# Performance work log

Hardware: AMD Instinct MI355X
Metric: run time of the kernel (lower is better)

## Reference

```python
import jax, jax.numpy as jnp
import numpy as np
import math

D_MODEL = 1024
N_HEADS = 16
D_K = 64
D_V = 64
B = 4
S = 1024


def setup_inputs() -> dict:
    key = jax.random.key(0)
    ks = jax.random.split(key, 11)
    # xavier-ish init scale for projections
    s_in = 1.0 / math.sqrt(D_MODEL)
    return {
        "queries": jax.random.normal(ks[0], (B, S, D_MODEL), jnp.float32),
        "keys": jax.random.normal(ks[1], (B, S, D_MODEL), jnp.float32),
        "values": jax.random.normal(ks[2], (B, S, D_MODEL), jnp.float32),
        "Wq": jax.random.normal(ks[3], (D_MODEL, N_HEADS * D_K), jnp.float32) * s_in,
        "bq": jnp.zeros((N_HEADS * D_K,), jnp.float32),
        "Wk": jax.random.normal(ks[4], (D_MODEL, N_HEADS * D_K), jnp.float32) * s_in,
        "bk": jnp.zeros((N_HEADS * D_K,), jnp.float32),
        "Wv": jax.random.normal(ks[5], (D_MODEL, N_HEADS * D_V), jnp.float32) * s_in,
        "bv": jnp.zeros((N_HEADS * D_V,), jnp.float32),
        "Wo": jax.random.normal(ks[6], (N_HEADS * D_V, D_MODEL), jnp.float32) * (1.0 / math.sqrt(N_HEADS * D_V)),
        "bo": jnp.zeros((D_MODEL,), jnp.float32),
    }


def reference(queries, keys, values, Wq, bq, Wk, bk, Wv, bv, Wo, bo):
    Bq, Sq, _ = queries.shape
    Sk = keys.shape[1]
    scale = 1.0 / math.sqrt(D_K)
    # projections -> [B, S, H, d]
    q = (queries @ Wq + bq).reshape(Bq, Sq, N_HEADS, D_K)
    k = (keys @ Wk + bk).reshape(Bq, Sk, N_HEADS, D_K)
    v = (values @ Wv + bv).reshape(Bq, Sk, N_HEADS, D_V)
    # scaled dot-product attention: scores [B, H, Sq, Sk]
    scores = jnp.einsum("bqhd,bkhd->bhqk", q, k) * scale
    attn = jax.nn.softmax(scores, axis=-1)
    # weighted values -> [B, Sq, H*D_V]
    out = jnp.einsum("bhqk,bkhd->bqhd", attn, v).reshape(Bq, Sq, N_HEADS * D_V)
    return out @ Wo + bo
```

## Files before the change

kernel.cpp:

```cpp
#include <hip/hip_runtime.h>

typedef __bf16 bf16;
typedef __attribute__((ext_vector_type(4))) __bf16 bf16x4;
typedef __attribute__((ext_vector_type(8))) __bf16 bf16x8;
typedef __attribute__((ext_vector_type(4))) float f32x4;

#define D_MODEL 1024
#define NH      16
#define DHEAD   64
#define BATCH   4
#define SLEN    1024
#define MROWS   (BATCH * SLEN)
#define C2SCALE 0.18033688f
#define SOFTMAX_OFF 20.0f

__device__ __forceinline__ void async_load16(const void* g, void* l) {
  __builtin_amdgcn_global_load_lds(
      (const __attribute__((address_space(1))) unsigned int*)g,
      (__attribute__((address_space(3))) unsigned int*)l,
      16, 0, 0);
}

__global__ __launch_bounds__(256) void cast3_kernel(
    const float* __restrict__ x0, const float* __restrict__ x1, const float* __restrict__ x2,
    bf16* __restrict__ y0, bf16* __restrict__ y1, bf16* __restrict__ y2, int n)
{
  const float* x; bf16* y;
  switch (blockIdx.y) {
    case 0: x = x0; y = y0; break;
    case 1: x = x1; y = y1; break;
    default: x = x2; y = y2; break;
  }
  int i = (blockIdx.x * 256 + threadIdx.x) * 4;
  if (i + 3 < n) {
    f32x4 v = *(const f32x4*)(x + i);
    bf16x4 o;
    o[0] = (bf16)v[0]; o[1] = (bf16)v[1]; o[2] = (bf16)v[2]; o[3] = (bf16)v[3];
    *(bf16x4*)(y + i) = o;
  }
}

__global__ __launch_bounds__(256) void transpose_cast4_kernel(
    const float* __restrict__ w0, const float* __restrict__ w1,
    const float* __restrict__ w2, const float* __restrict__ w3,
    bf16* __restrict__ t0, bf16* __restrict__ t1,
    bf16* __restrict__ t2, bf16* __restrict__ t3)
{
  __shared__ float tile[32][33];
  const float* W; bf16* T;
  switch (blockIdx.z) {
    case 0: W = w0; T = t0; break;
    case 1: W = w1; T = t1; break;
    case 2: W = w2; T = t2; break;
    default: W = w3; T = t3; break;
  }
  const int bx = blockIdx.x * 32, by = blockIdx.y * 32;
  const int tx = threadIdx.x & 31, ty = threadIdx.x >> 5;
  #pragma unroll
  for (int i = 0; i < 32; i += 8)
    tile[ty + i][tx] = W[(size_t)(by + ty + i) * 1024 + bx + tx];
  __syncthreads();
  #pragma unroll
  for (int i = 0; i < 32; i += 8)
    T[(size_t)(bx + ty + i) * 1024 + by + tx] = (bf16)tile[tx][ty + i];
}

__global__ __launch_bounds__(256) void proj_qkv_kernel(
    const bf16* __restrict__ Xq, const bf16* __restrict__ Xk, const bf16* __restrict__ Xv,
    const bf16* __restrict__ WqT, const bf16* __restrict__ WkT, const bf16* __restrict__ WvT,
    const float* __restrict__ bq, const float* __restrict__ bk, const float* __restrict__ bv,
    bf16* __restrict__ Qh, bf16* __restrict__ Kh, bf16* __restrict__ VTo)
{
  __shared__ bf16 As[128 * 32];
  __shared__ bf16 Bs[128 * 32];
  const int z = blockIdx.z;
  const bf16 *A, *BT; const float* bias;
  switch (z) {
    case 0: A = Xq; BT = WqT; bias = bq; break;
    case 1: A = Xk; BT = WkT; bias = bk; break;
    default: A = Xv; BT = WvT; bias = bv; break;
  }
  const int t = threadIdx.x;
  const int wave = t >> 6, lane = t & 63;
  const int quad = lane >> 4, l16 = lane & 15;
  const int wr = wave >> 1, wc = wave & 1;
  const int bM = blockIdx.y * 128, bN = blockIdx.x * 128;

  f32x4 acc[4][4] = {};

  for (int k0 = 0; k0 < D_MODEL; k0 += 32) {
    __syncthreads();
    #pragma unroll
    for (int i = 0; i < 2; ++i) {
      const int idx = i * 256 + t;
      const int row = idx >> 2, cg = idx & 3;
      async_load16(A  + (size_t)(bM + row) * D_MODEL + k0 + cg * 8,
                   As + (size_t)(i * 256 + wave * 64) * 8);
      async_load16(BT + (size_t)(bN + row) * D_MODEL + k0 + cg * 8,
                   Bs + (size_t)(i * 256 + wave * 64) * 8);
    }
    __syncthreads();

    bf16x8 af[4], bfr[4];
    #pragma unroll
    for (int i = 0; i < 4; ++i)
      af[i] = *(const bf16x8*)(As + (wr * 64 + i * 16 + l16) * 32 + quad * 8);
    #pragma unroll
    for (int j = 0; j < 4; ++j)
      bfr[j] = *(const bf16x8*)(Bs + (wc * 64 + j * 16 + l16) * 32 + quad * 8);
    #pragma unroll
    for (int i = 0; i < 4; ++i)
      #pragma unroll
      for (int j = 0; j < 4; ++j)
        acc[i][j] = __builtin_amdgcn_mfma_f32_16x16x32_bf16(af[i], bfr[j], acc[i][j], 0, 0, 0);
  }

  #pragma unroll
  for (int j = 0; j < 4; ++j) {
    const int col = bN + wc * 64 + j * 16 + l16;
    const int h = col >> 6, d = col & 63;
    const float bv_ = bias[col];
    #pragma unroll
    for (int i = 0; i < 4; ++i) {
      const int row0 = bM + wr * 64 + i * 16 + quad * 4;
      const int b = row0 >> 10, s0 = row0 & 1023;
      if (z == 0) {
        bf16* dst = Qh + ((size_t)(b * NH + h) * SLEN) * DHEAD;
        #pragma unroll
        for (int r = 0; r < 4; ++r)
          dst[(size_t)(s0 + r) * DHEAD + d] = (bf16)((acc[i][j][r] + bv_) * C2SCALE);
      } else if (z == 1) {
        bf16* dst = Kh + ((size_t)(b * NH + h) * SLEN) * DHEAD;
        #pragma unroll
        for (int r = 0; r < 4; ++r)
          dst[(size_t)(s0 + r) * DHEAD + d] = (bf16)(acc[i][j][r] + bv_);
      } else {
        bf16x4 pv;
        #pragma unroll
        for (int r = 0; r < 4; ++r) pv[r] = (bf16)(acc[i][j][r] + bv_);
        *(bf16x4*)(VTo + ((size_t)(b * NH + h) * DHEAD + d) * SLEN + s0) = pv;
      }
    }
  }
}

__global__ __launch_bounds__(256) void out_proj_kernel(
    const bf16* __restrict__ AO, const bf16* __restrict__ WoT,
    const float* __restrict__ bo, float* __restrict__ Out)
{
  __shared__ bf16 As[64 * 32];
  __shared__ bf16 Bs[128 * 32];
  const int t = threadIdx.x;
  const int wave = t >> 6, lane = t & 63;
  const int quad = lane >> 4, l16 = lane & 15;
  const int wr = wave >> 1, wc = wave & 1;
  const int bM = blockIdx.y * 64, bN = blockIdx.x * 128;

  f32x4 acc[2][4] = {};

  for (int k0 = 0; k0 < D_MODEL; k0 += 32) {
    __syncthreads();
    {
      const int row = t >> 2, cg = t & 3;
      async_load16(AO  + (size_t)(bM + row) * D_MODEL + k0 + cg * 8,
                   As + (size_t)(wave * 64) * 8);
    }
    #pragma unroll
    for (int i = 0; i < 2; ++i) {
      const int idx = i * 256 + t;
      const int row = idx >> 2, cg = idx & 3;
      async_load16(WoT + (size_t)(bN + row) * D_MODEL + k0 + cg * 8,
                   Bs + (size_t)(i * 256 + wave * 64) * 8);
    }
    __syncthreads();

    bf16x8 af[2], bfr[4];
    #pragma unroll
    for (int i = 0; i < 2; ++i)
      af[i] = *(const bf16x8*)(As + (wr * 32 + i * 16 + l16) * 32 + quad * 8);
    #pragma unroll
    for (int j = 0; j < 4; ++j)
      bfr[j] = *(const bf16x8*)(Bs + (wc * 64 + j * 16 + l16) * 32 + quad * 8);
    #pragma unroll
    for (int i = 0; i < 2; ++i)
      #pragma unroll
      for (int j = 0; j < 4; ++j)
        acc[i][j] = __builtin_amdgcn_mfma_f32_16x16x32_bf16(af[i], bfr[j], acc[i][j], 0, 0, 0);
  }

  #pragma unroll
  for (int j = 0; j < 4; ++j) {
    const int col = bN + wc * 64 + j * 16 + l16;
    const float bv_ = bo[col];
    #pragma unroll
    for (int i = 0; i < 2; ++i) {
      const int row0 = bM + wr * 32 + i * 16 + quad * 4;
      #pragma unroll
      for (int r = 0; r < 4; ++r)
        Out[(size_t)(row0 + r) * D_MODEL + col] = acc[i][j][r] + bv_;
    }
  }
}

#define OCS  68
#define WSEG (32 * OCS)
__global__ __launch_bounds__(256) void attn_kernel(
    const bf16* __restrict__ Q, const bf16* __restrict__ K,
    const bf16* __restrict__ VT, bf16* __restrict__ O)
{
  const int bh = blockIdx.y;
  const int b = bh >> 4, h = bh & 15;
  const int qBase = blockIdx.x * 32;

  __shared__ float smem_f[4 * WSEG + 4 * 32];

  const int t = threadIdx.x;
  const int wave = t >> 6, lane = t & 63;
  const int quad = lane >> 4, l16 = lane & 15;
  const int kt0 = wave * 256;

  const bf16* qb = Q  + (size_t)bh * SLEN * DHEAD;
  const bf16* kb = K  + (size_t)bh * SLEN * DHEAD;
  const bf16* vb = VT + (size_t)bh * DHEAD * SLEN;

  bf16x8 qa[2][2];
  #pragma unroll
  for (int g = 0; g < 2; ++g) {
    const bf16* qr = qb + (size_t)(qBase + g * 16 + l16) * DHEAD;
    qa[g][0] = *(const bf16x8*)(qr + quad * 8);
    qa[g][1] = *(const bf16x8*)(qr + 32 + quad * 8);
  }

  f32x4 o_acc[2][4] = {};
  float rs[2][4] = {};

  bf16* Pw = (bf16*)smem_f + wave * (2 * 16 * 72);

  bf16x8 kf0[4], kf1[4];
  #pragma unroll
  for (int jn = 0; jn < 4; ++jn) {
    const bf16* kr = kb + (size_t)(kt0 + jn * 16 + l16) * DHEAD;
    kf0[jn] = *(const bf16x8*)(kr + quad * 8);
    kf1[jn] = *(const bf16x8*)(kr + 32 + quad * 8);
  }

  #pragma unroll
  for (int tt = 0; tt < 4; ++tt) {
    const int kt = kt0 + tt * 64;

    bf16x8 vf0[4], vf1[4];
    #pragma unroll
    for (int jn = 0; jn < 4; ++jn) {
      const bf16* vr = vb + (size_t)(jn * 16 + l16) * SLEN + kt;
      vf0[jn] = *(const bf16x8*)(vr + quad * 8);
      vf1[jn] = *(const bf16x8*)(vr + 32 + quad * 8);
    }

    f32x4 s[2][4] = {};
    __builtin_amdgcn_s_setprio(1);
    #pragma unroll
    for (int jn = 0; jn < 4; ++jn) {
      s[0][jn] = __builtin_amdgcn_mfma_f32_16x16x32_bf16(qa[0][0], kf0[jn], s[0][jn], 0, 0, 0);
      s[0][jn] = __builtin_amdgcn_mfma_f32_16x16x32_bf16(qa[0][1], kf1[jn], s[0][jn], 0, 0, 0);
      s[1][jn] = __builtin_amdgcn_mfma_f32_16x16x32_bf16(qa[1][0], kf0[jn], s[1][jn], 0, 0, 0);
      s[1][jn] = __builtin_amdgcn_mfma_f32_16x16x32_bf16(qa[1][1], kf1[jn], s[1][jn], 0, 0, 0);
    }
    __builtin_amdgcn_s_setprio(0);

    #pragma unroll
    for (int g = 0; g < 2; ++g) {
      bf16* ps = Pw + g * (16 * 72);
      #pragma unroll
      for (int jn = 0; jn < 4; ++jn)
        #pragma unroll
        for (int r = 0; r < 4; ++r) {
          float p = __builtin_amdgcn_exp2f(s[g][jn][r] - SOFTMAX_OFF);
          rs[g][r] += p;
          ps[(quad * 4 + r) * 72 + jn * 16 + l16] = (bf16)p;
        }
    }

    bf16x8 kn0[4], kn1[4];
    if (tt < 3) {
      #pragma unroll
      for (int jn = 0; jn < 4; ++jn) {
        const bf16* kr = kb + (size_t)(kt + 64 + jn * 16 + l16) * DHEAD;
        kn0[jn] = *(const bf16x8*)(kr + quad * 8);
        kn1[jn] = *(const bf16x8*)(kr + 32 + quad * 8);
      }
    }

    bf16x8 pa[2][2];
    #pragma unroll
    for (int g = 0; g < 2; ++g) {
      const bf16* ps = Pw + g * (16 * 72);
      pa[g][0] = *(const bf16x8*)(&ps[l16 * 72 + quad * 8]);
      pa[g][1] = *(const bf16x8*)(&ps[l16 * 72 + 32 + quad * 8]);
    }

    __builtin_amdgcn_s_setprio(1);
    #pragma unroll
    for (int jn = 0; jn < 4; ++jn) {
      o_acc[0][jn] = __builtin_amdgcn_mfma_f32_16x16x32_bf16(pa[0][0], vf0[jn], o_acc[0][jn], 0, 0, 0);
      o_acc[0][jn] = __builtin_amdgcn_mfma_f32_16x16x32_bf16(pa[0][1], vf1[jn], o_acc[0][jn], 0, 0, 0);
      o_acc[1][jn] = __builtin_amdgcn_mfma_f32_16x16x32_bf16(pa[1][0], vf0[jn], o_acc[1][jn], 0, 0, 0);
      o_acc[1][jn] = __builtin_amdgcn_mfma_f32_16x16x32_bf16(pa[1][1], vf1[jn], o_acc[1][jn], 0, 0, 0);
    }
    __builtin_amdgcn_s_setprio(0);

    if (tt < 3) {
      #pragma unroll
      for (int jn = 0; jn < 4; ++jn) { kf0[jn] = kn0[jn]; kf1[jn] = kn1[jn]; }
    }
  }

  #pragma unroll
  for (int g = 0; g < 2; ++g)
    #pragma unroll
    for (int r = 0; r < 4; ++r) {
      float v = rs[g][r];
      #pragma unroll
      for (int off = 1; off < 16; off <<= 1)
        v += __shfl_xor(v, off);
      rs[g][r] = v;
    }

  __syncthreads();

  float* oc = smem_f + wave * WSEG;
  float* lc = smem_f + 4 * WSEG + wave * 32;
  #pragma unroll
  for (int g = 0; g < 2; ++g) {
    #pragma unroll
    for (int jn = 0; jn < 4; ++jn)
      #pragma unroll
      for (int r = 0; r < 4; ++r)
        oc[(g * 16 + quad * 4 + r) * OCS + jn * 16 + l16] = o_acc[g][jn][r];
    if (l16 == 0)
      #pragma unroll
      for (int r = 0; r < 4; ++r)
        lc[g * 16 + quad * 4 + r] = rs[g][r];
  }
  __syncthreads();

  const int row = wave * 8 + (lane >> 3);
  const int dbase = (lane & 7) * 8;
  float ltot = smem_f[4 * WSEG + row] + smem_f[4 * WSEG + 32 + row] +
               smem_f[4 * WSEG + 64 + row] + smem_f[4 * WSEG + 96 + row];
  f32x4 a0 = {}, a1 = {};
  #pragma unroll
  for (int w = 0; w < 4; ++w) {
    a0 += *(const f32x4*)&smem_f[w * WSEG + row * OCS + dbase];
    a1 += *(const f32x4*)&smem_f[w * WSEG + row * OCS + dbase + 4];
  }
  const float inv = 1.0f / ltot;
  bf16x8 ov;
  #pragma unroll
  for (int e = 0; e < 4; ++e) { ov[e] = (bf16)(a0[e] * inv); ov[e + 4] = (bf16)(a1[e] * inv); }
  bf16* op = O + ((size_t)b * SLEN + qBase + row) * D_MODEL + h * DHEAD + dbase;
  *(bf16x8*)op = ov;
}

extern "C" void kernel_launch(void* const* d_in, const int* in_sizes, int n_in,
                              void* d_out, int out_size, void* d_ws, size_t ws_size,
                              hipStream_t stream) {
  const float* xq = (const float*)d_in[0];
  const float* xk = (const float*)d_in[1];
  const float* xv = (const float*)d_in[2];
  const float* Wq = (const float*)d_in[3];
  const float* bq = (const float*)d_in[4];
  const float* Wk = (const float*)d_in[5];
  const float* bk = (const float*)d_in[6];
  const float* Wv = (const float*)d_in[7];
  const float* bv = (const float*)d_in[8];
  const float* Wo = (const float*)d_in[9];
  const float* bo = (const float*)d_in[10];
  float* out = (float*)d_out;

  const size_t NX = (size_t)MROWS * D_MODEL;
  const size_t NW = (size_t)D_MODEL * D_MODEL;

  char* ws = (char*)d_ws;
  bf16* AO  = (bf16*)ws;  ws += NX * 2;
  bf16* WoT = (bf16*)ws;  ws += NW * 2;
  bf16* Xq  = (bf16*)ws;  ws += NX * 2;
  bf16* Xk  = (bf16*)ws;  ws += NX * 2;
  bf16* Xv  = (bf16*)ws;  ws += NX * 2;
  bf16* WqT = (bf16*)ws;  ws += NW * 2;
  bf16* WkT = (bf16*)ws;  ws += NW * 2;
  bf16* WvT = (bf16*)ws;  ws += NW * 2;
  bf16* Qh  = (bf16*)ws;  ws += NX * 2;
  bf16* Kh  = (bf16*)ws;  ws += NX * 2;
  bf16* VTb = (bf16*)ws;  ws += NX * 2;

  cast3_kernel<<<dim3(4096, 3), 256, 0, stream>>>(xq, xk, xv, Xq, Xk, Xv, (int)NX);
  transpose_cast4_kernel<<<dim3(32, 32, 4), 256, 0, stream>>>(Wq, Wk, Wv, Wo, WqT, WkT, WvT, WoT);
  proj_qkv_kernel<<<dim3(8, 32, 3), 256, 0, stream>>>(Xq, Xk, Xv, WqT, WkT, WvT, bq, bk, bv, Qh, Kh, VTb);
  attn_kernel<<<dim3(32, 64), 256, 0, stream>>>(Qh, Kh, VTb, AO);
  out_proj_kernel<<<dim3(8, 64), 256, 0, stream>>>(AO, WoT, bo, out);
}
```

Baseline: 243.7 us.

## Double-buffer GEMM LDS loads, fuse prep kernels, remap attention blocks per XCD

```diff
diff --git a/kernel.cpp b/kernel.cpp
--- a/kernel.cpp
+++ b/kernel.cpp
@@ -21,48 +21,51 @@
       16, 0, 0);
 }
 
-__global__ __launch_bounds__(256) void cast3_kernel(
+__global__ __launch_bounds__(256) void prep_kernel(
     const float* __restrict__ x0, const float* __restrict__ x1, const float* __restrict__ x2,
-    bf16* __restrict__ y0, bf16* __restrict__ y1, bf16* __restrict__ y2, int n)
-{
-  const float* x; bf16* y;
-  switch (blockIdx.y) {
-    case 0: x = x0; y = y0; break;
-    case 1: x = x1; y = y1; break;
-    default: x = x2; y = y2; break;
-  }
-  int i = (blockIdx.x * 256 + threadIdx.x) * 4;
-  if (i + 3 < n) {
-    f32x4 v = *(const f32x4*)(x + i);
-    bf16x4 o;
-    o[0] = (bf16)v[0]; o[1] = (bf16)v[1]; o[2] = (bf16)v[2]; o[3] = (bf16)v[3];
-    *(bf16x4*)(y + i) = o;
-  }
-}
-
-__global__ __launch_bounds__(256) void transpose_cast4_kernel(
+    bf16* __restrict__ y0, bf16* __restrict__ y1, bf16* __restrict__ y2, int n,
     const float* __restrict__ w0, const float* __restrict__ w1,
     const float* __restrict__ w2, const float* __restrict__ w3,
     bf16* __restrict__ t0, bf16* __restrict__ t1,
     bf16* __restrict__ t2, bf16* __restrict__ t3)
 {
   __shared__ float tile[32][33];
-  const float* W; bf16* T;
-  switch (blockIdx.z) {
-    case 0: W = w0; T = t0; break;
-    case 1: W = w1; T = t1; break;
-    case 2: W = w2; T = t2; break;
-    default: W = w3; T = t3; break;
-  }
-  const int bx = blockIdx.x * 32, by = blockIdx.y * 32;
-  const int tx = threadIdx.x & 31, ty = threadIdx.x >> 5;
-  #pragma unroll
-  for (int i = 0; i < 32; i += 8)
-    tile[ty + i][tx] = W[(size_t)(by + ty + i) * 1024 + bx + tx];
-  __syncthreads();
-  #pragma unroll
-  for (int i = 0; i < 32; i += 8)
-    T[(size_t)(bx + ty + i) * 1024 + by + tx] = (bf16)tile[tx][ty + i];
+  const int bid = blockIdx.x;
+  if (bid < 3 * 4096) {
+    const int z = bid >> 12, bx = bid & 4095;
+    const float* x; bf16* y;
+    switch (z) {
+      case 0: x = x0; y = y0; break;
+      case 1: x = x1; y = y1; break;
+      default: x = x2; y = y2; break;
+    }
+    int i = (bx * 256 + threadIdx.x) * 4;
+    if (i + 3 < n) {
+      f32x4 v = *(const f32x4*)(x + i);
+      bf16x4 o;
+      o[0] = (bf16)v[0]; o[1] = (bf16)v[1]; o[2] = (bf16)v[2]; o[3] = (bf16)v[3];
+      *(bf16x4*)(y + i) = o;
+    }
+  } else {
+    const int r = bid - 3 * 4096;
+    const int z = r >> 10, rr = r & 1023;
+    const float* W; bf16* T;
+    switch (z) {
+      case 0: W = w0; T = t0; break;
+      case 1: W = w1; T = t1; break;
+      case 2: W = w2; T = t2; break;
+      default: W = w3; T = t3; break;
+    }
+    const int bx = (rr & 31) * 32, by = (rr >> 5) * 32;
+    const int tx = threadIdx.x & 31, ty = threadIdx.x >> 5;
+    #pragma unroll
+    for (int i = 0; i < 32; i += 8)
+      tile[ty + i][tx] = W[(size_t)(by + ty + i) * 1024 + bx + tx];
+    __syncthreads();
+    #pragma unroll
+    for (int i = 0; i < 32; i += 8)
+      T[(size_t)(bx + ty + i) * 1024 + by + tx] = (bf16)tile[tx][ty + i];
+  }
 }
 
 __global__ __launch_bounds__(256) void proj_qkv_kernel(
@@ -71,8 +74,8 @@
     const float* __restrict__ bq, const float* __restrict__ bk, const float* __restrict__ bv,
     bf16* __restrict__ Qh, bf16* __restrict__ Kh, bf16* __restrict__ VTo)
 {
-  __shared__ bf16 As[128 * 32];
-  __shared__ bf16 Bs[128 * 32];
+  __shared__ bf16 As[2][128 * 32];
+  __shared__ bf16 Bs[2][128 * 32];
   const int z = blockIdx.z;
   const bf16 *A, *BT; const float* bias;
   switch (z) {
@@ -88,31 +91,41 @@
 
   f32x4 acc[4][4] = {};
 
-  for (int k0 = 0; k0 < D_MODEL; k0 += 32) {
-    __syncthreads();
+  auto stage = [&](int buf, int k0) {
     #pragma unroll
     for (int i = 0; i < 2; ++i) {
       const int idx = i * 256 + t;
       const int row = idx >> 2, cg = idx & 3;
       async_load16(A  + (size_t)(bM + row) * D_MODEL + k0 + cg * 8,
-                   As + (size_t)(i * 256 + wave * 64) * 8);
+                   &As[buf][(i * 256 + wave * 64) * 8]);
       async_load16(BT + (size_t)(bN + row) * D_MODEL + k0 + cg * 8,
-                   Bs + (size_t)(i * 256 + wave * 64) * 8);
-    }
-    __syncthreads();
-
+                   &Bs[buf][(i * 256 + wave * 64) * 8]);
+    }
+  };
+  auto compute = [&](int buf) {
     bf16x8 af[4], bfr[4];
     #pragma unroll
     for (int i = 0; i < 4; ++i)
-      af[i] = *(const bf16x8*)(As + (wr * 64 + i * 16 + l16) * 32 + quad * 8);
+      af[i] = *(const bf16x8*)(&As[buf][(wr * 64 + i * 16 + l16) * 32 + quad * 8]);
     #pragma unroll
     for (int j = 0; j < 4; ++j)
-      bfr[j] = *(const bf16x8*)(Bs + (wc * 64 + j * 16 + l16) * 32 + quad * 8);
+      bfr[j] = *(const bf16x8*)(&Bs[buf][(wc * 64 + j * 16 + l16) * 32 + quad * 8]);
     #pragma unroll
     for (int i = 0; i < 4; ++i)
       #pragma unroll
       for (int j = 0; j < 4; ++j)
         acc[i][j] = __builtin_amdgcn_mfma_f32_16x16x32_bf16(af[i], bfr[j], acc[i][j], 0, 0, 0);
+  };
+
+  stage(0, 0);
+  __syncthreads();
+  for (int k0 = 0; k0 < D_MODEL; k0 += 64) {
+    stage(1, k0 + 32);
+    compute(0);
+    __syncthreads();
+    if (k0 + 64 < D_MODEL) stage(0, k0 + 64);
+    compute(1);
+    __syncthreads();
   }
 
   #pragma unroll
@@ -148,8 +161,8 @@
     const bf16* __restrict__ AO, const bf16* __restrict__ WoT,
     const float* __restrict__ bo, float* __restrict__ Out)
 {
-  __shared__ bf16 As[64 * 32];
-  __shared__ bf16 Bs[128 * 32];
+  __shared__ bf16 As[2][64 * 32];
+  __shared__ bf16 Bs[2][128 * 32];
   const int t = threadIdx.x;
   const int wave = t >> 6, lane = t & 63;
   const int quad = lane >> 4, l16 = lane & 15;
@@ -158,34 +171,44 @@
 
   f32x4 acc[2][4] = {};
 
-  for (int k0 = 0; k0 < D_MODEL; k0 += 32) {
-    __syncthreads();
+  auto stage = [&](int buf, int k0) {
     {
       const int row = t >> 2, cg = t & 3;
-      async_load16(AO  + (size_t)(bM + row) * D_MODEL + k0 + cg * 8,
-                   As + (size_t)(wave * 64) * 8);
+      async_load16(AO + (size_t)(bM + row) * D_MODEL + k0 + cg * 8,
+                   &As[buf][(wave * 64) * 8]);
     }
     #pragma unroll
     for (int i = 0; i < 2; ++i) {
       const int idx = i * 256 + t;
       const int row = idx >> 2, cg = idx & 3;
       async_load16(WoT + (size_t)(bN + row) * D_MODEL + k0 + cg * 8,
-                   Bs + (size_t)(i * 256 + wave * 64) * 8);
-    }
-    __syncthreads();
-
+                   &Bs[buf][(i * 256 + wave * 64) * 8]);
+    }
+  };
+  auto compute = [&](int buf) {
     bf16x8 af[2], bfr[4];
     #pragma unroll
     for (int i = 0; i < 2; ++i)
-      af[i] = *(const bf16x8*)(As + (wr * 32 + i * 16 + l16) * 32 + quad * 8);
+      af[i] = *(const bf16x8*)(&As[buf][(wr * 32 + i * 16 + l16) * 32 + quad * 8]);
     #pragma unroll
     for (int j = 0; j < 4; ++j)
-      bfr[j] = *(const bf16x8*)(Bs + (wc * 64 + j * 16 + l16) * 32 + quad * 8);
+      bfr[j] = *(const bf16x8*)(&Bs[buf][(wc * 64 + j * 16 + l16) * 32 + quad * 8]);
     #pragma unroll
     for (int i = 0; i < 2; ++i)
       #pragma unroll
       for (int j = 0; j < 4; ++j)
         acc[i][j] = __builtin_amdgcn_mfma_f32_16x16x32_bf16(af[i], bfr[j], acc[i][j], 0, 0, 0);
+  };
+
+  stage(0, 0);
+  __syncthreads();
+  for (int k0 = 0; k0 < D_MODEL; k0 += 64) {
+    stage(1, k0 + 32);
+    compute(0);
+    __syncthreads();
+    if (k0 + 64 < D_MODEL) stage(0, k0 + 64);
+    compute(1);
+    __syncthreads();
   }
 
   #pragma unroll
@@ -208,9 +231,11 @@
     const bf16* __restrict__ Q, const bf16* __restrict__ K,
     const bf16* __restrict__ VT, bf16* __restrict__ O)
 {
-  const int bh = blockIdx.y;
+  const int lin = blockIdx.x + (blockIdx.y << 5);
+  const int xcd = lin & 7, idx = lin >> 3;
+  const int bh = xcd * 8 + (idx >> 5);
+  const int qBase = (idx & 31) << 5;
   const int b = bh >> 4, h = bh & 15;
-  const int qBase = blockIdx.x * 32;
 
   __shared__ float smem_f[4 * WSEG + 4 * 32];
 
@@ -255,6 +280,7 @@
       vf0[jn] = *(const bf16x8*)(vr + quad * 8);
       vf1[jn] = *(const bf16x8*)(vr + 32 + quad * 8);
     }
+    __builtin_amdgcn_sched_barrier(0);
 
     f32x4 s[2][4] = {};
     __builtin_amdgcn_s_setprio(1);
@@ -288,6 +314,7 @@
         kn0[jn] = *(const bf16x8*)(kr + quad * 8);
         kn1[jn] = *(const bf16x8*)(kr + 32 + quad * 8);
       }
+      __builtin_amdgcn_sched_barrier(0);
     }
 
     bf16x8 pa[2][2];
@@ -393,8 +420,8 @@
   bf16* Kh  = (bf16*)ws;  ws += NX * 2;
   bf16* VTb = (bf16*)ws;  ws += NX * 2;
 
-  cast3_kernel<<<dim3(4096, 3), 256, 0, stream>>>(xq, xk, xv, Xq, Xk, Xv, (int)NX);
-  transpose_cast4_kernel<<<dim3(32, 32, 4), 256, 0, stream>>>(Wq, Wk, Wv, Wo, WqT, WkT, WvT, WoT);
+  prep_kernel<<<dim3(3 * 4096 + 4 * 1024), 256, 0, stream>>>(
+      xq, xk, xv, Xq, Xk, Xv, (int)NX, Wq, Wk, Wv, Wo, WqT, WkT, WvT, WoT);
   proj_qkv_kernel<<<dim3(8, 32, 3), 256, 0, stream>>>(Xq, Xk, Xv, WqT, WkT, WvT, bq, bk, bv, Qh, Kh, VTb);
   attn_kernel<<<dim3(32, 64), 256, 0, stream>>>(Qh, Kh, VTb, AO);
   out_proj_kernel<<<dim3(8, 64), 256, 0, stream>>>(AO, WoT, bo, out);
```

After: 244.8 us. No clear change (+0.4%).
